# Kernel tuning notes

Hardware: AMD Instinct MI355X
Metric: run time of the kernel (lower is better)

The kernel has to match this reference:

```python
import jax, jax.numpy as jnp
import numpy as np

U_NUM, I_NUM, F_DIM, N_EDGES, BATCH = 50000, 20000, 64, 1000000, 131072
T = 1.0  # temperature

def setup_inputs() -> dict:
    key = jax.random.key(0)
    ks = jax.random.split(key, 16)
    return {
        'embed_user': jax.random.normal(ks[0], (U_NUM, F_DIM), jnp.float32) * 0.01,
        'embed_item': jax.random.normal(ks[1], (I_NUM, F_DIM), jnp.float32) * 0.01,
        'old_U_emb': jax.random.normal(ks[2], (U_NUM, F_DIM), jnp.float32),
        'old_I_emb': jax.random.normal(ks[3], (I_NUM, F_DIM), jnp.float32),
        'edge_rows': jax.random.randint(ks[4], (N_EDGES,), 0, U_NUM, jnp.int32),
        'edge_cols': jax.random.randint(ks[5], (N_EDGES,), 0, I_NUM, jnp.int32),
        'ui_vals': jax.random.uniform(ks[6], (N_EDGES,), jnp.float32),
        'iu_vals': jax.random.uniform(ks[7], (N_EDGES,), jnp.float32),
        'user': jax.random.randint(ks[8], (BATCH,), 0, U_NUM, jnp.int32),
        'item_i': jax.random.randint(ks[9], (BATCH,), 0, U_NUM, jnp.int32),
        'item_j': jax.random.randint(ks[10], (BATCH,), 0, U_NUM, jnp.int32),
        'degree_U': jax.random.uniform(ks[11], (BATCH,), jnp.float32),
        'item_z_U': jax.random.randint(ks[12], (BATCH,), 0, U_NUM, jnp.int32),
        'user_': jax.random.randint(ks[13], (BATCH,), 0, I_NUM, jnp.int32),
        'item_i_': jax.random.randint(ks[14], (BATCH,), 0, I_NUM, jnp.int32),
        'item_j_': jax.random.randint(ks[15], (BATCH,), 0, I_NUM, jnp.int32),
        'degree_I': jax.random.uniform(jax.random.fold_in(key, 99), (BATCH,), jnp.float32),
        'item_z_I': jax.random.randint(jax.random.fold_in(key, 98), (BATCH,), 0, I_NUM, jnp.int32),
    }

def _spmm_ui(vals, rows, cols, item_emb):
    # (U x I sparse) @ item_emb -> [U, F]
    return jax.ops.segment_sum(vals[:, None] * item_emb[cols], rows, num_segments=U_NUM)

def _spmm_iu(vals, rows, cols, user_emb):
    # (I x U sparse) @ user_emb -> [I, F]
    return jax.ops.segment_sum(vals[:, None] * user_emb[rows], cols, num_segments=I_NUM)

def _contrastive(idx_u, idx_i, idx_j, degree, num, old_emb, gcn_emb):
    u = old_emb[idx_u]            # [B, F]
    pi = gcn_emb[idx_i]           # [B, F]
    pj = gcn_emb[idx_j]           # [B, F]
    si = jnp.sum(u * pi, axis=-1) / T
    sj = jnp.sum(u * pj, axis=-1) / T
    # -log(exp(si) / (exp(sj) + exp(si))) = logaddexp(si, sj) - si  (stable form)
    log_ratio = si - jnp.logaddexp(si, sj)
    return -jnp.sum(log_ratio * degree) / num

def reference(embed_user, embed_item, old_U_emb, old_I_emb, ui_vals, iu_vals,
              degree_U, degree_I, edge_rows, edge_cols,
              user, item_i, item_j, item_z_U, user_, item_i_, item_j_, item_z_I):
    u0, i0 = embed_user, embed_item
    u1 = _spmm_ui(ui_vals, edge_rows, edge_cols, i0)
    i1 = _spmm_iu(iu_vals, edge_rows, edge_cols, u0)
    u2 = _spmm_ui(ui_vals, edge_rows, edge_cols, i1)
    i2 = _spmm_iu(iu_vals, edge_rows, edge_cols, u1)
    u3 = _spmm_ui(ui_vals, edge_rows, edge_cols, i2)
    i3 = _spmm_iu(iu_vals, edge_rows, edge_cols, u2)
    gcn_u = u0 + 0.5 * u1 + (1.0 / 3.0) * u2 + 0.25 * u3
    gcn_i = i0 + 0.5 * i1 + (1.0 / 3.0) * i2 + 0.25 * i3
    loss = _contrastive(user, item_i, item_j, degree_U, U_NUM, old_U_emb, gcn_u)
    loss = loss + _contrastive(user_, item_i_, item_j_, degree_I, I_NUM, old_I_emb, gcn_i)
    return loss
```

## Files before the change

kernel.cpp:

```cpp
#include <hip/hip_runtime.h>

#define U_NUM 50000
#define I_NUM 20000
#define F_DIM 64
#define N_EDGES 1000000
#define BATCH 131072

#define P_U 25
#define P_I 20
#define CAPP_U 45056
#define CAPP_I 55296
#define FP_U 200
#define FP_I 160
#define CAPF_U 5632
#define CAPF_I 6912
#define BRU 40
#define BRI 50
#define P1B 977

#if defined(__has_builtin)
#if __has_builtin(__builtin_amdgcn_cvt_pk_f32_fp8) && __has_builtin(__builtin_amdgcn_cvt_pk_fp8_f32)
#define HW_FP8 1
#endif
#endif

typedef float v2f __attribute__((ext_vector_type(2)));

__device__ __forceinline__ void dec4(unsigned u, float* f) {
#ifdef HW_FP8
    v2f lo = __builtin_amdgcn_cvt_pk_f32_fp8((int)u, false);
    v2f hi = __builtin_amdgcn_cvt_pk_f32_fp8((int)u, true);
    f[0] = lo.x; f[1] = lo.y; f[2] = hi.x; f[3] = hi.y;
#else
    #pragma unroll
    for (int i = 0; i < 4; i++) {
        unsigned v = (u >> (8 * i)) & 0xFFu;
        unsigned s = v >> 7, e = (v >> 3) & 15u, m = v & 7u;
        float mag = (e == 0) ? (float)m * 0.001953125f
                             : __uint_as_float(((e + 120u) << 23) | (m << 20));
        f[i] = s ? -mag : mag;
    }
#endif
}

#ifndef HW_FP8
__device__ __forceinline__ unsigned char enc1(float x) {
    unsigned s = (__float_as_uint(x) >> 31) << 7;
    float a = fabsf(x);
    if (a >= 448.f) return (unsigned char)(s | 0x7E);
    if (a < 0.015625f) {
        int m = __float2int_rn(a * 512.f);
        if (m >= 8) return (unsigned char)(s | 0x08);
        return (unsigned char)(s | m);
    }
    unsigned au = __float_as_uint(a);
    au += 0x7FFFFu + ((au >> 20) & 1u);
    int e = (int)(au >> 23) - 127;
    if (e > 8) return (unsigned char)(s | 0x7E);
    return (unsigned char)(s | ((unsigned)(e + 7) << 3) | ((au >> 20) & 7u));
}
#endif

__device__ __forceinline__ unsigned enc4(float a, float b, float c, float d) {
#ifdef HW_FP8
    int v = __builtin_amdgcn_cvt_pk_fp8_f32(a, b, 0, false);
    v = __builtin_amdgcn_cvt_pk_fp8_f32(c, d, v, true);
    return (unsigned)v;
#else
    return (unsigned)enc1(a) | ((unsigned)enc1(b) << 8)
         | ((unsigned)enc1(c) << 16) | ((unsigned)enc1(d) << 24);
#endif
}

__device__ __forceinline__ unsigned short f2b(float f) {
    unsigned b = __float_as_uint(f);
    b += 0x7FFFu + ((b >> 16) & 1u);
    return (unsigned short)(b >> 16);
}

#define N_EU 800000
#define N_EI 320000
#define N_OU 800000
#define N_OI 320000
__global__ void pass1_cvt(const int* __restrict__ rows, const int* __restrict__ cols,
                          const float* __restrict__ uiv, const float* __restrict__ iuv,
                          int* __restrict__ pcurU, int* __restrict__ pcurI,
                          int2* __restrict__ cbufU, int2* __restrict__ cbufI,
                          const float* __restrict__ eU, const float* __restrict__ eI,
                          const float* __restrict__ oU, const float* __restrict__ oI,
                          unsigned* __restrict__ e8U, unsigned* __restrict__ e8I,
                          unsigned* __restrict__ o8U, unsigned* __restrict__ o8I)
{
    if (blockIdx.x >= P1B) {
        int idx = (blockIdx.x - P1B) * 256 + threadIdx.x;
        const float* s; unsigned* d; int off; float sc;
        if (idx < N_EU)                        { s = eU; d = e8U; off = idx; sc = 128.f; }
        else if (idx < N_EU + N_EI)            { s = eI; d = e8I; off = idx - N_EU; sc = 128.f; }
        else if (idx < N_EU + N_EI + N_OU)     { s = oU; d = o8U; off = idx - N_EU - N_EI; sc = 1.f; }
        else if (idx < N_EU + N_EI + N_OU + N_OI) { s = oI; d = o8I; off = idx - N_EU - N_EI - N_OU; sc = 1.f; }
        else return;
        float4 v = ((const float4*)s)[off];
        d[off] = enc4(v.x * sc, v.y * sc, v.z * sc, v.w * sc);
        return;
    }

    __shared__ int histU[32], histI[32];
    __shared__ int lbaseU[32], lbaseI[32];
    __shared__ int deltaU[32], deltaI[32];
    __shared__ int totU, totI;
    __shared__ int2 recU[1024], recI[1024];
    __shared__ unsigned char pidU[1024], pidI[1024];

    if (threadIdx.x < 32) { histU[threadIdx.x] = 0; histI[threadIdx.x] = 0; }
    __syncthreads();

    int base = blockIdx.x * 1024;
    int r[4], c[4], lpU[4], lpI[4];
    float vu[4], vi[4];
    #pragma unroll
    for (int i = 0; i < 4; i++) {
        int e = base + threadIdx.x + i * 256;
        if (e < N_EDGES) {
            r[i] = rows[e]; c[i] = cols[e];
            vu[i] = uiv[e]; vi[i] = iuv[e];
            lpU[i] = atomicAdd(&histU[r[i] >> 11], 1);
            lpI[i] = atomicAdd(&histI[c[i] >> 10], 1);
        } else {
            lpU[i] = -1; lpI[i] = -1; r[i] = 0; c[i] = 0; vu[i] = 0.f; vi[i] = 0.f;
        }
    }
    __syncthreads();

    int lane = threadIdx.x & 63;
    int w    = threadIdx.x >> 6;
    if (w == 0) {
        int h = (lane < 32) ? histU[lane] : 0;
        int res = (lane < 32 && h) ? atomicAdd(&pcurU[lane], h) : 0;
        int inc = h;
        #pragma unroll
        for (int off = 1; off < 32; off <<= 1) {
            int t = __shfl_up(inc, off, 64);
            if (lane >= off) inc += t;
        }
        if (lane < 32) {
            int lb = inc - h;
            lbaseU[lane] = lb;
            deltaU[lane] = lane * CAPP_U + res - lb;
            if (lane == 31) totU = inc;
        }
    } else if (w == 1) {
        int h = (lane < 32) ? histI[lane] : 0;
        int res = (lane < 32 && h) ? atomicAdd(&pcurI[lane], h) : 0;
        int inc = h;
        #pragma unroll
        for (int off = 1; off < 32; off <<= 1) {
            int t = __shfl_up(inc, off, 64);
            if (lane >= off) inc += t;
        }
        if (lane < 32) {
            int lb = inc - h;
            lbaseI[lane] = lb;
            deltaI[lane] = lane * CAPP_I + res - lb;
            if (lane == 31) totI = inc;
        }
    }
    __syncthreads();

    #pragma unroll
    for (int i = 0; i < 4; i++) {
        if (lpU[i] >= 0) {
            int p = r[i] >> 11;
            int slot = lbaseU[p] + lpU[i];
            int2 rec;
            rec.x = (int)(((unsigned)c[i] << 16) | (unsigned)r[i]);
            rec.y = __float_as_int(vu[i]);
            recU[slot] = rec;
            pidU[slot] = (unsigned char)p;

            p = c[i] >> 10;
            slot = lbaseI[p] + lpI[i];
            rec.x = (int)(((unsigned)r[i] << 16) | (unsigned)c[i]);
            rec.y = __float_as_int(vi[i]);
            recI[slot] = rec;
            pidI[slot] = (unsigned char)p;
        }
    }
    __syncthreads();

    for (int t = threadIdx.x; t < totU; t += 256) {
        int p = pidU[t];
        int a = deltaU[p] + t;
        if (a < (p + 1) * CAPP_U) cbufU[a] = recU[t];
    }
    for (int t = threadIdx.x; t < totI; t += 256) {
        int p = pidI[t];
        int a = deltaI[p] + t;
        if (a < (p + 1) * CAPP_I) cbufI[a] = recI[t];
    }
}

__global__ void refine(const int* __restrict__ pcurU, const int2* __restrict__ cbufU,
                       int* __restrict__ fcurU, int2* __restrict__ fbufU,
                       const int* __restrict__ pcurI, const int2* __restrict__ cbufI,
                       int* __restrict__ fcurI, int2* __restrict__ fbufI)
{
    const int* pcur; const int2* cbuf; int* fcur; int2* fbuf;
    int p, b, br, capp, capf, shift;
    if (blockIdx.x < P_U * BRU) {
        pcur = pcurU; cbuf = cbufU; fcur = fcurU; fbuf = fbufU;
        p = blockIdx.x / BRU; b = blockIdx.x % BRU; br = BRU;
        capp = CAPP_U; capf = CAPF_U; shift = 8;
    } else {
        int q = blockIdx.x - P_U * BRU;
        pcur = pcurI; cbuf = cbufI; fcur = fcurI; fbuf = fbufI;
        p = q / BRI; b = q % BRI; br = BRI;
        capp = CAPP_I; capf = CAPF_I; shift = 7;
    }
    int n = min(pcur[p], capp);
    const int2* src = cbuf + (size_t)p * capp;

    __shared__ int hist[8], lbase[8], delta[8];
    __shared__ int tot;
    __shared__ int2 rec[1024];
    __shared__ unsigned char pid[1024];

    for (int base = b * 1024; base < n; base += br * 1024) {
        __syncthreads();
        if (threadIdx.x < 8) hist[threadIdx.x] = 0;
        __syncthreads();
        int2 rr[4]; int ff[4], lp[4];
        #pragma unroll
        for (int i = 0; i < 4; i++) {
            int t = base + i * 256 + threadIdx.x;
            if (t < n) {
                rr[i] = src[t];
                ff[i] = (int)((((unsigned)rr[i].x & 0xFFFFu) >> shift) & 7u);
                lp[i] = atomicAdd(&hist[ff[i]], 1);
            } else lp[i] = -1;
        }
        __syncthreads();
        if ((threadIdx.x >> 6) == 0) {
            int lane = threadIdx.x & 63;
            int h = (lane < 8) ? hist[lane] : 0;
            int res = (lane < 8 && h) ? atomicAdd(&fcur[p * 8 + lane], h) : 0;
            int inc = h;
            #pragma unroll
            for (int off = 1; off < 8; off <<= 1) {
                int t = __shfl_up(inc, off, 64);
                if (lane >= off) inc += t;
            }
            if (lane < 8) {
                int lb = inc - h;
                lbase[lane] = lb;
                delta[lane] = (p * 8 + lane) * capf + res - lb;
                if (lane == 7) tot = inc;
            }
        }
        __syncthreads();
        #pragma unroll
        for (int i = 0; i < 4; i++) {
            if (lp[i] >= 0) {
                int slot = lbase[ff[i]] + lp[i];
                rec[slot] = rr[i];
                pid[slot] = (unsigned char)ff[i];
            }
        }
        __syncthreads();
        for (int t = threadIdx.x; t < tot; t += 256) {
            int f2 = pid[t];
            int a = delta[f2] + t;
            if (a < (p * 8 + f2 + 1) * capf) fbuf[a] = rec[t];
        }
    }
}

__global__ void sort_csr(const int* __restrict__ fcurU, const int2* __restrict__ fbufU,
                         int* __restrict__ ptrU, int* __restrict__ cntU, unsigned* __restrict__ edgesU,
                         const int* __restrict__ fcurI, const int2* __restrict__ fbufI,
                         int* __restrict__ ptrI, int* __restrict__ cntI, unsigned* __restrict__ edgesI)
{
    __shared__ int hist[256], scan[256], curs[256];
    __shared__ int gbase_s;

    const int* fcur; const int2* fbuf; int* ptr; int* cnt; unsigned* edges;
    int fp, bins, capf, nrow;
    if (blockIdx.x < FP_U) {
        fcur = fcurU; fbuf = fbufU; ptr = ptrU; cnt = cntU; edges = edgesU;
        fp = blockIdx.x; bins = 256; capf = CAPF_U; nrow = U_NUM;
    } else {
        fcur = fcurI; fbuf = fbufI; ptr = ptrI; cnt = cntI; edges = edgesI;
        fp = blockIdx.x - FP_U; bins = 128; capf = CAPF_I; nrow = I_NUM;
    }

    if (threadIdx.x == 0) gbase_s = 0;
    for (int i = threadIdx.x; i < bins; i += 256) hist[i] = 0;
    __syncthreads();

    int contrib = ((int)threadIdx.x < fp) ? min(fcur[threadIdx.x], capf) : 0;
    #pragma unroll
    for (int off = 32; off > 0; off >>= 1) contrib += __shfl_down(contrib, off, 64);
    if ((threadIdx.x & 63) == 0 && contrib) atomicAdd(&gbase_s, contrib);

    int n = min(fcur[fp], capf);
    const int2* src = fbuf + (size_t)fp * capf;
    int mask = bins - 1;

    for (int t = threadIdx.x; t < n; t += 256) {
        int dst = src[t].x & 0xFFFF;
        atomicAdd(&hist[dst & mask], 1);
    }
    __syncthreads();

    int v = ((int)threadIdx.x < bins) ? hist[threadIdx.x] : 0;
    scan[threadIdx.x] = v;
    __syncthreads();
    for (int off = 1; off < 256; off <<= 1) {
        int t = ((int)threadIdx.x >= off) ? scan[threadIdx.x - off] : 0;
        __syncthreads();
        scan[threadIdx.x] += t;
        __syncthreads();
    }
    int ex = scan[threadIdx.x] - v;
    curs[threadIdx.x] = ex;
    __syncthreads();
    int gbase = gbase_s;

    if ((int)threadIdx.x < bins) {
        int row = fp * bins + threadIdx.x;
        if (row < nrow) {
            ptr[row] = gbase + ex;
            cnt[row] = v;
        }
    }

    for (int t = threadIdx.x; t < n; t += 256) {
        int2 r = src[t];
        int dst = r.x & 0xFFFF;
        int pos = atomicAdd(&curs[dst & mask], 1);
        unsigned rec = ((unsigned)f2b(__int_as_float(r.y)) << 16)
                     | ((unsigned)r.x >> 16);
        edges[gbase + pos] = rec;
    }
}

template <int MODE>
__global__ void spmm_level(const int* __restrict__ ptrU, const int* __restrict__ cntU,
                           const unsigned* __restrict__ edgesU, const unsigned* __restrict__ srcU,
                           unsigned* __restrict__ dstU,
                           const unsigned* __restrict__ l0U, const unsigned* __restrict__ l1U,
                           const unsigned* __restrict__ l2U, unsigned* __restrict__ g8U,
                           const int* __restrict__ ptrI, const int* __restrict__ cntI,
                           const unsigned* __restrict__ edgesI, const unsigned* __restrict__ srcI,
                           unsigned* __restrict__ dstI,
                           const unsigned* __restrict__ l0I, const unsigned* __restrict__ l1I,
                           const unsigned* __restrict__ l2I, unsigned* __restrict__ g8I)
{
    int wave = (blockIdx.x * blockDim.x + threadIdx.x) >> 6;
    bool isU = wave < U_NUM;
    int row = isU ? wave : wave - U_NUM;
    if (!isU && row >= I_NUM) return;

    const int*  ptr   = isU ? ptrU   : ptrI;
    const int*  cnt   = isU ? cntU   : cntI;
    const unsigned* edges = isU ? edgesU : edgesI;
    const unsigned* semb  = isU ? srcU   : srcI;

    int lane = threadIdx.x & 63;
    int sub  = lane >> 4;
    int q    = lane & 15;
    int begin = __builtin_amdgcn_readfirstlane(ptr[row]);
    int len   = __builtin_amdgcn_readfirstlane(cnt[row]);
    const unsigned* erow = edges + begin;

    float4 a0 = make_float4(0.f, 0.f, 0.f, 0.f);
    float4 a1 = make_float4(0.f, 0.f, 0.f, 0.f);
    float4 a2 = make_float4(0.f, 0.f, 0.f, 0.f);
    float4 a3 = make_float4(0.f, 0.f, 0.f, 0.f);
    int k = sub;
    for (; k + 12 < len; k += 16) {
        unsigned r0 = erow[k];
        unsigned r1 = erow[k + 4];
        unsigned r2 = erow[k + 8];
        unsigned r3 = erow[k + 12];
        unsigned x0 = semb[((size_t)(r0 & 0xFFFFu) << 4) + q];
        unsigned x1 = semb[((size_t)(r1 & 0xFFFFu) << 4) + q];
        unsigned x2 = semb[((size_t)(r2 & 0xFFFFu) << 4) + q];
        unsigned x3 = semb[((size_t)(r3 & 0xFFFFu) << 4) + q];
        float v0 = __uint_as_float(r0 & 0xFFFF0000u);
        float v1 = __uint_as_float(r1 & 0xFFFF0000u);
        float v2 = __uint_as_float(r2 & 0xFFFF0000u);
        float v3 = __uint_as_float(r3 & 0xFFFF0000u);
        float f0[4], f1[4], f2[4], f3[4];
        dec4(x0, f0); dec4(x1, f1); dec4(x2, f2); dec4(x3, f3);
        a0.x += v0 * f0[0]; a0.y += v0 * f0[1]; a0.z += v0 * f0[2]; a0.w += v0 * f0[3];
        a1.x += v1 * f1[0]; a1.y += v1 * f1[1]; a1.z += v1 * f1[2]; a1.w += v1 * f1[3];
        a2.x += v2 * f2[0]; a2.y += v2 * f2[1]; a2.z += v2 * f2[2]; a2.w += v2 * f2[3];
        a3.x += v3 * f3[0]; a3.y += v3 * f3[1]; a3.z += v3 * f3[2]; a3.w += v3 * f3[3];
    }
    for (; k < len; k += 4) {
        unsigned r0 = erow[k];
        unsigned x0 = semb[((size_t)(r0 & 0xFFFFu) << 4) + q];
        float v0 = __uint_as_float(r0 & 0xFFFF0000u);
        float f0[4];
        dec4(x0, f0);
        a0.x += v0 * f0[0]; a0.y += v0 * f0[1]; a0.z += v0 * f0[2]; a0.w += v0 * f0[3];
    }
    float4 acc;
    acc.x = (a0.x + a1.x) + (a2.x + a3.x);
    acc.y = (a0.y + a1.y) + (a2.y + a3.y);
    acc.z = (a0.z + a1.z) + (a2.z + a3.z);
    acc.w = (a0.w + a1.w) + (a2.w + a3.w);

    acc.x += __shfl_xor(acc.x, 16, 64);
    acc.y += __shfl_xor(acc.y, 16, 64);
    acc.z += __shfl_xor(acc.z, 16, 64);
    acc.w += __shfl_xor(acc.w, 16, 64);
    acc.x += __shfl_xor(acc.x, 32, 64);
    acc.y += __shfl_xor(acc.y, 32, 64);
    acc.z += __shfl_xor(acc.z, 32, 64);
    acc.w += __shfl_xor(acc.w, 32, 64);

    if (sub == 0) {
        size_t ro = ((size_t)row << 4) + q;
        if (MODE < 2) {
            unsigned* dst = isU ? dstU : dstI;
            dst[ro] = enc4(acc.x, acc.y, acc.z, acc.w);
        } else {
            const unsigned* l0 = isU ? l0U : l0I;
            const unsigned* l1 = isU ? l1U : l1I;
            const unsigned* l2 = isU ? l2U : l2I;
            unsigned* g8       = isU ? g8U : g8I;
            float e[4], b[4], c[4];
            dec4(l0[ro], e); dec4(l1[ro], b); dec4(l2[ro], c);
            const float third = 1.f / 3.f;
            float gx = 0.125f * (e[0] + 0.5f * b[0] + third * c[0] + 0.25f * acc.x);
            float gy = 0.125f * (e[1] + 0.5f * b[1] + third * c[1] + 0.25f * acc.y);
            float gz = 0.125f * (e[2] + 0.5f * b[2] + third * c[2] + 0.25f * acc.z);
            float gw = 0.125f * (e[3] + 0.5f * b[3] + third * c[3] + 0.25f * acc.w);
            g8[ro] = enc4(gx, gy, gz, gw);
        }
    }
}

__device__ __forceinline__ float dotq(const float* a, const float* b) {
    return a[0] * b[0] + a[1] * b[1] + a[2] * b[2] + a[3] * b[3];
}

__global__ void __launch_bounds__(256, 2)
contrastive_both(const unsigned* __restrict__ oldU, const unsigned* __restrict__ gcnU,
                 const int* __restrict__ userU, const int* __restrict__ iiU,
                 const int* __restrict__ ijU, const float* __restrict__ degU,
                 const unsigned* __restrict__ oldI, const unsigned* __restrict__ gcnI,
                 const int* __restrict__ userI, const int* __restrict__ iiI,
                 const int* __restrict__ ijI, const float* __restrict__ degI,
                 float* __restrict__ out)
{
    int lane = threadIdx.x & 63;
    int sub  = lane >> 4;
    int ql   = lane & 15;
    int qg = (blockIdx.x * blockDim.x + threadIdx.x) >> 4;
    int s0 = qg << 2;

    int sel = ql >> 2, so = s0 + (ql & 3);
    const int* pu = (sel == 0) ? (userU + so) : (sel == 1) ? (iiU + so)
                  : (sel == 2) ? (ijU + so)   : ((const int*)degU + so);
    const int* pi = (sel == 0) ? (userI + so) : (sel == 1) ? (iiI + so)
                  : (sel == 2) ? (ijI + so)   : ((const int*)degI + so);
    int idxU = *pu;
    int idxI = *pi;

    int qb = sub << 4;
    unsigned Au[4], Ai[4], Aj[4], Bu[4], Bi[4], Bj[4];
    #pragma unroll
    for (int t = 0; t < 4; t++) {
        int uU = __shfl(idxU, qb + t, 64);
        int iU = __shfl(idxU, qb + 4 + t, 64);
        int jU = __shfl(idxU, qb + 8 + t, 64);
        int uI = __shfl(idxI, qb + t, 64);
        int iI = __shfl(idxI, qb + 4 + t, 64);
        int jI = __shfl(idxI, qb + 8 + t, 64);
        Au[t] = oldU[((size_t)uU << 4) + ql];
        Ai[t] = gcnU[((size_t)iU << 4) + ql];
        Aj[t] = gcnU[((size_t)jU << 4) + ql];
        Bu[t] = oldI[((size_t)uI << 4) + ql];
        Bi[t] = gcnI[((size_t)iI << 4) + ql];
        Bj[t] = gcnI[((size_t)jI << 4) + ql];
    }

    float siU[4], sjU[4], siI[4], sjI[4];
    #pragma unroll
    for (int t = 0; t < 4; t++) {
        float fu[4], fi[4], fj[4];
        dec4(Au[t], fu); dec4(Ai[t], fi); dec4(Aj[t], fj);
        siU[t] = dotq(fu, fi); sjU[t] = dotq(fu, fj);
        dec4(Bu[t], fu); dec4(Bi[t], fi); dec4(Bj[t], fj);
        siI[t] = dotq(fu, fi); sjI[t] = dotq(fu, fj);
    }

    #pragma unroll
    for (int off = 1; off < 16; off <<= 1) {
        #pragma unroll
        for (int t = 0; t < 4; t++) {
            siU[t] += __shfl_xor(siU[t], off, 64);
            sjU[t] += __shfl_xor(sjU[t], off, 64);
            siI[t] += __shfl_xor(siI[t], off, 64);
            sjI[t] += __shfl_xor(sjI[t], off, 64);
        }
    }

    int t3 = ql & 3;
    bool isI = (ql & 4) != 0;
    float si = isI ? siI[t3] : siU[t3];
    float sj = isI ? sjI[t3] : sjU[t3];
    float dg = __int_as_float(__shfl(isI ? idxI : idxU, qb + 12 + t3, 64));
    float inv = isI ? (1.f / I_NUM) : (1.f / U_NUM);

    const float S = 0.0625f;
    si *= S; sj *= S;
    float m = fmaxf(si, sj);
    float lse = m + logf(expf(si - m) + expf(sj - m));
    float acc = (ql < 8) ? -(si - lse) * dg * inv : 0.f;

    #pragma unroll
    for (int off = 32; off > 0; off >>= 1) acc += __shfl_down(acc, off, 64);
    __shared__ float wsum[4];
    if (lane == 0) wsum[threadIdx.x >> 6] = acc;
    __syncthreads();
    if (threadIdx.x == 0)
        atomicAdd(out, wsum[0] + wsum[1] + wsum[2] + wsum[3]);
}

extern "C" void kernel_launch(void* const* d_in, const int* in_sizes, int n_in,
                              void* d_out, int out_size, void* d_ws, size_t ws_size,
                              hipStream_t stream)
{
    const float* embed_user = (const float*)d_in[0];
    const float* embed_item = (const float*)d_in[1];
    const float* old_U      = (const float*)d_in[2];
    const float* old_I      = (const float*)d_in[3];
    const int*   erow       = (const int*)d_in[4];
    const int*   ecol       = (const int*)d_in[5];
    const float* ui_vals    = (const float*)d_in[6];
    const float* iu_vals    = (const float*)d_in[7];
    const int*   user       = (const int*)d_in[8];
    const int*   item_i     = (const int*)d_in[9];
    const int*   item_j     = (const int*)d_in[10];
    const float* degU       = (const float*)d_in[11];
    const int*   user_      = (const int*)d_in[13];
    const int*   item_i_    = (const int*)d_in[14];
    const int*   item_j_    = (const int*)d_in[15];
    const float* degI       = (const float*)d_in[16];

    const size_t UF = (size_t)U_NUM * F_DIM;
    const size_t IF = (size_t)I_NUM * F_DIM;
    const size_t CREC = (size_t)P_U * CAPP_U + (size_t)P_I * CAPP_I;

    int2*  cbufU  = (int2*)d_ws;
    int2*  cbufI  = cbufU + (size_t)P_U * CAPP_U;
    unsigned* edgesU = (unsigned*)d_ws;
    unsigned* edgesI = edgesU + N_EDGES;
    int2*  fbufU  = (int2*)d_ws + CREC;
    int2*  fbufI  = fbufU + (size_t)FP_U * CAPF_U;
    char* cur = (char*)d_ws + 2 * CREC * sizeof(int2);
    unsigned* e8U = (unsigned*)cur; cur += UF;
    unsigned* e8I = (unsigned*)cur; cur += IF;
    unsigned* o8U = (unsigned*)cur; cur += UF;
    unsigned* o8I = (unsigned*)cur; cur += IF;
    unsigned* u1_8 = (unsigned*)cur; cur += UF;
    unsigned* u2_8 = (unsigned*)cur; cur += UF;
    unsigned* i1_8 = (unsigned*)cur; cur += IF;
    unsigned* i2_8 = (unsigned*)cur; cur += IF;
    unsigned* g8U  = (unsigned*)cur; cur += UF;
    unsigned* g8I  = (unsigned*)cur; cur += IF;
    int* pcurU = (int*)cur;
    int* pcurI = pcurU + 32;
    int* fcurU = pcurI + 32;
    int* fcurI = fcurU + 256;
    int* ptrU  = fcurI + 256;
    int* cntUa = ptrU + U_NUM;
    int* ptrI  = cntUa + U_NUM;
    int* cntIa = ptrI + I_NUM;

    dim3 blk(256);
    const int cv_blocks  = (N_EU + N_EI + N_OU + N_OI + 255) / 256;
    const int p1_blocks  = P1B + cv_blocks;
    const int rf_blocks  = P_U * BRU + P_I * BRI;
    const int st_blocks  = FP_U + FP_I;
    const int spmm_blocks = (U_NUM + I_NUM) / 4;

    hipMemsetAsync(pcurU, 0, 576 * sizeof(int), stream);
    hipMemsetAsync(d_out, 0, sizeof(float), stream);

    pass1_cvt<<<p1_blocks, blk, 0, stream>>>(erow, ecol, ui_vals, iu_vals,
                                             pcurU, pcurI, cbufU, cbufI,
                                             embed_user, embed_item, old_U, old_I,
                                             e8U, e8I, o8U, o8I);
    refine<<<rf_blocks, blk, 0, stream>>>(pcurU, cbufU, fcurU, fbufU,
                                          pcurI, cbufI, fcurI, fbufI);
    sort_csr<<<st_blocks, blk, 0, stream>>>(fcurU, fbufU, ptrU, cntUa, edgesU,
                                            fcurI, fbufI, ptrI, cntIa, edgesI);

    spmm_level<0><<<spmm_blocks, blk, 0, stream>>>(
        ptrU, cntUa, edgesU, e8I, u1_8, nullptr, nullptr, nullptr, nullptr,
        ptrI, cntIa, edgesI, e8U, i1_8, nullptr, nullptr, nullptr, nullptr);
    spmm_level<1><<<spmm_blocks, blk, 0, stream>>>(
        ptrU, cntUa, edgesU, i1_8, u2_8, nullptr, nullptr, nullptr, nullptr,
        ptrI, cntIa, edgesI, u1_8, i2_8, nullptr, nullptr, nullptr, nullptr);
    spmm_level<2><<<spmm_blocks, blk, 0, stream>>>(
        ptrU, cntUa, edgesU, i2_8, nullptr, e8U, u1_8, u2_8, g8U,
        ptrI, cntIa, edgesI, u2_8, nullptr, e8I, i1_8, i2_8, g8I);

    contrastive_both<<<2048, blk, 0, stream>>>(o8U, g8U, user, item_i, item_j, degU,
                                               o8I, g8I, user_, item_i_, item_j_, degI,
                                               (float*)d_out);
}
```

Baseline: 307.1 us.

## Replace two-pass coarse/refine edge bucketing with single-pass fine binning

Merges the coarse partition pass and the refine pass into one kernel. Each block takes an 8192-edge tile, builds a 256-bin shared-memory histogram, scans it, and scatters records straight into the fine bins. This drops the intermediate coarse buffer, which was written once and read back, and removes one kernel launch. The fp8 conversion work moves to a grid-stride loop over 512 blocks. The cost is fewer, larger blocks with 72KB of shared memory each, which lowers occupancy, plus more shared-memory atomic contention.

New measurement: 304.8 us. No clear change (-0.8%).

```diff
diff --git a/kernel.cpp b/kernel.cpp
--- a/kernel.cpp
+++ b/kernel.cpp
@@ -6,17 +6,14 @@
 #define N_EDGES 1000000
 #define BATCH 131072
 
-#define P_U 25
-#define P_I 20
-#define CAPP_U 45056
-#define CAPP_I 55296
 #define FP_U 200
 #define FP_I 160
 #define CAPF_U 5632
 #define CAPF_I 6912
-#define BRU 40
-#define BRI 50
-#define P1B 977
+#define TILE 8192
+#define NBU 123
+#define NBI 123
+#define CVB 512
 
 #if defined(__has_builtin)
 #if __has_builtin(__builtin_amdgcn_cvt_pk_f32_fp8) && __has_builtin(__builtin_amdgcn_cvt_pk_fp8_f32)
@@ -82,195 +79,89 @@
 #define N_EI 320000
 #define N_OU 800000
 #define N_OI 320000
-__global__ void pass1_cvt(const int* __restrict__ rows, const int* __restrict__ cols,
-                          const float* __restrict__ uiv, const float* __restrict__ iuv,
-                          int* __restrict__ pcurU, int* __restrict__ pcurI,
-                          int2* __restrict__ cbufU, int2* __restrict__ cbufI,
-                          const float* __restrict__ eU, const float* __restrict__ eI,
-                          const float* __restrict__ oU, const float* __restrict__ oI,
-                          unsigned* __restrict__ e8U, unsigned* __restrict__ e8I,
-                          unsigned* __restrict__ o8U, unsigned* __restrict__ o8I)
+#define CVT_TOT (N_EU + N_EI + N_OU + N_OI)
+__global__ void build_fine(const int* __restrict__ rows, const int* __restrict__ cols,
+                           const float* __restrict__ uiv, const float* __restrict__ iuv,
+                           int* __restrict__ fcurU, int2* __restrict__ fbufU,
+                           int* __restrict__ fcurI, int2* __restrict__ fbufI,
+                           const float* __restrict__ eU, const float* __restrict__ eI,
+                           const float* __restrict__ oU, const float* __restrict__ oI,
+                           unsigned* __restrict__ e8U, unsigned* __restrict__ e8I,
+                           unsigned* __restrict__ o8U, unsigned* __restrict__ o8I)
 {
-    if (blockIdx.x >= P1B) {
-        int idx = (blockIdx.x - P1B) * 256 + threadIdx.x;
-        const float* s; unsigned* d; int off; float sc;
-        if (idx < N_EU)                        { s = eU; d = e8U; off = idx; sc = 128.f; }
-        else if (idx < N_EU + N_EI)            { s = eI; d = e8I; off = idx - N_EU; sc = 128.f; }
-        else if (idx < N_EU + N_EI + N_OU)     { s = oU; d = o8U; off = idx - N_EU - N_EI; sc = 1.f; }
-        else if (idx < N_EU + N_EI + N_OU + N_OI) { s = oI; d = o8I; off = idx - N_EU - N_EI - N_OU; sc = 1.f; }
-        else return;
-        float4 v = ((const float4*)s)[off];
-        d[off] = enc4(v.x * sc, v.y * sc, v.z * sc, v.w * sc);
+    if (blockIdx.x >= NBU + NBI) {
+        for (int idx = (blockIdx.x - NBU - NBI) * 256 + threadIdx.x;
+             idx < CVT_TOT; idx += CVB * 256) {
+            const float* s; unsigned* d; int off; float sc;
+            if (idx < N_EU)                      { s = eU; d = e8U; off = idx; sc = 128.f; }
+            else if (idx < N_EU + N_EI)          { s = eI; d = e8I; off = idx - N_EU; sc = 128.f; }
+            else if (idx < N_EU + N_EI + N_OU)   { s = oU; d = o8U; off = idx - N_EU - N_EI; sc = 1.f; }
+            else                                 { s = oI; d = o8I; off = idx - N_EU - N_EI - N_OU; sc = 1.f; }
+            float4 v = ((const float4*)s)[off];
+            d[off] = enc4(v.x * sc, v.y * sc, v.z * sc, v.w * sc);
+        }
         return;
     }
 
-    __shared__ int histU[32], histI[32];
-    __shared__ int lbaseU[32], lbaseI[32];
-    __shared__ int deltaU[32], deltaI[32];
-    __shared__ int totU, totI;
-    __shared__ int2 recU[1024], recI[1024];
-    __shared__ unsigned char pidU[1024], pidI[1024];
-
-    if (threadIdx.x < 32) { histU[threadIdx.x] = 0; histI[threadIdx.x] = 0; }
-    __syncthreads();
-
-    int base = blockIdx.x * 1024;
-    int r[4], c[4], lpU[4], lpI[4];
-    float vu[4], vi[4];
-    #pragma unroll
-    for (int i = 0; i < 4; i++) {
-        int e = base + threadIdx.x + i * 256;
-        if (e < N_EDGES) {
-            r[i] = rows[e]; c[i] = cols[e];
-            vu[i] = uiv[e]; vi[i] = iuv[e];
-            lpU[i] = atomicAdd(&histU[r[i] >> 11], 1);
-            lpI[i] = atomicAdd(&histI[c[i] >> 10], 1);
-        } else {
-            lpU[i] = -1; lpI[i] = -1; r[i] = 0; c[i] = 0; vu[i] = 0.f; vi[i] = 0.f;
-        }
-    }
-    __syncthreads();
-
-    int lane = threadIdx.x & 63;
-    int w    = threadIdx.x >> 6;
-    if (w == 0) {
-        int h = (lane < 32) ? histU[lane] : 0;
-        int res = (lane < 32 && h) ? atomicAdd(&pcurU[lane], h) : 0;
-        int inc = h;
-        #pragma unroll
-        for (int off = 1; off < 32; off <<= 1) {
-            int t = __shfl_up(inc, off, 64);
-            if (lane >= off) inc += t;
-        }
-        if (lane < 32) {
-            int lb = inc - h;
-            lbaseU[lane] = lb;
-            deltaU[lane] = lane * CAPP_U + res - lb;
-            if (lane == 31) totU = inc;
-        }
-    } else if (w == 1) {
-        int h = (lane < 32) ? histI[lane] : 0;
-        int res = (lane < 32 && h) ? atomicAdd(&pcurI[lane], h) : 0;
-        int inc = h;
-        #pragma unroll
-        for (int off = 1; off < 32; off <<= 1) {
-            int t = __shfl_up(inc, off, 64);
-            if (lane >= off) inc += t;
-        }
-        if (lane < 32) {
-            int lb = inc - h;
-            lbaseI[lane] = lb;
-            deltaI[lane] = lane * CAPP_I + res - lb;
-            if (lane == 31) totI = inc;
-        }
-    }
-    __syncthreads();
-
-    #pragma unroll
-    for (int i = 0; i < 4; i++) {
-        if (lpU[i] >= 0) {
-            int p = r[i] >> 11;
-            int slot = lbaseU[p] + lpU[i];
-            int2 rec;
-            rec.x = (int)(((unsigned)c[i] << 16) | (unsigned)r[i]);
-            rec.y = __float_as_int(vu[i]);
-            recU[slot] = rec;
-            pidU[slot] = (unsigned char)p;
-
-            p = c[i] >> 10;
-            slot = lbaseI[p] + lpI[i];
-            rec.x = (int)(((unsigned)r[i] << 16) | (unsigned)c[i]);
-            rec.y = __float_as_int(vi[i]);
-            recI[slot] = rec;
-            pidI[slot] = (unsigned char)p;
-        }
-    }
-    __syncthreads();
-
-    for (int t = threadIdx.x; t < totU; t += 256) {
-        int p = pidU[t];
-        int a = deltaU[p] + t;
-        if (a < (p + 1) * CAPP_U) cbufU[a] = recU[t];
-    }
-    for (int t = threadIdx.x; t < totI; t += 256) {
-        int p = pidI[t];
-        int a = deltaI[p] + t;
-        if (a < (p + 1) * CAPP_I) cbufI[a] = recI[t];
-    }
-}
-
-__global__ void refine(const int* __restrict__ pcurU, const int2* __restrict__ cbufU,
-                       int* __restrict__ fcurU, int2* __restrict__ fbufU,
-                       const int* __restrict__ pcurI, const int2* __restrict__ cbufI,
-                       int* __restrict__ fcurI, int2* __restrict__ fbufI)
-{
-    const int* pcur; const int2* cbuf; int* fcur; int2* fbuf;
-    int p, b, br, capp, capf, shift;
-    if (blockIdx.x < P_U * BRU) {
-        pcur = pcurU; cbuf = cbufU; fcur = fcurU; fbuf = fbufU;
-        p = blockIdx.x / BRU; b = blockIdx.x % BRU; br = BRU;
-        capp = CAPP_U; capf = CAPF_U; shift = 8;
-    } else {
-        int q = blockIdx.x - P_U * BRU;
-        pcur = pcurI; cbuf = cbufI; fcur = fcurI; fbuf = fbufI;
-        p = q / BRI; b = q % BRI; br = BRI;
-        capp = CAPP_I; capf = CAPF_I; shift = 7;
-    }
-    int n = min(pcur[p], capp);
-    const int2* src = cbuf + (size_t)p * capp;
-
-    __shared__ int hist[8], lbase[8], delta[8];
-    __shared__ int tot;
-    __shared__ int2 rec[1024];
-    __shared__ unsigned char pid[1024];
-
-    for (int base = b * 1024; base < n; base += br * 1024) {
+    __shared__ int2 rec[TILE];
+    __shared__ unsigned char pid[TILE];
+    __shared__ int hist[256], scan[256], curs[256], delta[256];
+
+    bool isU = blockIdx.x < NBU;
+    int tb = isU ? blockIdx.x : blockIdx.x - NBU;
+    int n0 = tb * TILE;
+    int n  = min(TILE, N_EDGES - n0);
+    int bins  = isU ? FP_U : FP_I;
+    int capf  = isU ? CAPF_U : CAPF_I;
+    int shift = isU ? 8 : 7;
+    int* fcur = isU ? fcurU : fcurI;
+    int2* fbuf = isU ? fbufU : fbufI;
+    const int* keys = isU ? rows : cols;
+    const int* srcs = isU ? cols : rows;
+    const float* vals = isU ? uiv : iuv;
+
+    hist[threadIdx.x] = 0;
+    __syncthreads();
+
+    for (int t = threadIdx.x; t < n; t += 256)
+        atomicAdd(&hist[keys[n0 + t] >> shift], 1);
+    __syncthreads();
+
+    int v = hist[threadIdx.x];
+    scan[threadIdx.x] = v;
+    __syncthreads();
+    for (int off = 1; off < 256; off <<= 1) {
+        int t = ((int)threadIdx.x >= off) ? scan[threadIdx.x - off] : 0;
         __syncthreads();
-        if (threadIdx.x < 8) hist[threadIdx.x] = 0;
+        scan[threadIdx.x] += t;
         __syncthreads();
-        int2 rr[4]; int ff[4], lp[4];
-        #pragma unroll
-        for (int i = 0; i < 4; i++) {
-            int t = base + i * 256 + threadIdx.x;
-            if (t < n) {
-                rr[i] = src[t];
-                ff[i] = (int)((((unsigned)rr[i].x & 0xFFFFu) >> shift) & 7u);
-                lp[i] = atomicAdd(&hist[ff[i]], 1);
-            } else lp[i] = -1;
-        }
-        __syncthreads();
-        if ((threadIdx.x >> 6) == 0) {
-            int lane = threadIdx.x & 63;
-            int h = (lane < 8) ? hist[lane] : 0;
-            int res = (lane < 8 && h) ? atomicAdd(&fcur[p * 8 + lane], h) : 0;
-            int inc = h;
-            #pragma unroll
-            for (int off = 1; off < 8; off <<= 1) {
-                int t = __shfl_up(inc, off, 64);
-                if (lane >= off) inc += t;
-            }
-            if (lane < 8) {
-                int lb = inc - h;
-                lbase[lane] = lb;
-                delta[lane] = (p * 8 + lane) * capf + res - lb;
-                if (lane == 7) tot = inc;
-            }
-        }
-        __syncthreads();
-        #pragma unroll
-        for (int i = 0; i < 4; i++) {
-            if (lp[i] >= 0) {
-                int slot = lbase[ff[i]] + lp[i];
-                rec[slot] = rr[i];
-                pid[slot] = (unsigned char)ff[i];
-            }
-        }
-        __syncthreads();
-        for (int t = threadIdx.x; t < tot; t += 256) {
-            int f2 = pid[t];
-            int a = delta[f2] + t;
-            if (a < (p * 8 + f2 + 1) * capf) fbuf[a] = rec[t];
-        }
+    }
+    int lbase = scan[threadIdx.x] - v;
+    curs[threadIdx.x] = lbase;
+    if ((int)threadIdx.x < bins) {
+        int res = v ? atomicAdd(&fcur[threadIdx.x], v) : 0;
+        delta[threadIdx.x] = threadIdx.x * capf + res - lbase;
+    }
+    __syncthreads();
+
+    for (int t = threadIdx.x; t < n; t += 256) {
+        int key = keys[n0 + t];
+        int src = srcs[n0 + t];
+        float vv = vals[n0 + t];
+        int b = key >> shift;
+        int slot = atomicAdd(&curs[b], 1);
+        int2 r;
+        r.x = (int)(((unsigned)src << 16) | (unsigned)key);
+        r.y = __float_as_int(vv);
+        rec[slot] = r;
+        pid[slot] = (unsigned char)b;
+    }
+    __syncthreads();
+
+    for (int t = threadIdx.x; t < n; t += 256) {
+        int b = pid[t];
+        int a = delta[b] + t;
+        if (a < (b + 1) * capf) fbuf[a] = rec[t];
     }
 }
 
@@ -553,15 +444,14 @@
 
     const size_t UF = (size_t)U_NUM * F_DIM;
     const size_t IF = (size_t)I_NUM * F_DIM;
-    const size_t CREC = (size_t)P_U * CAPP_U + (size_t)P_I * CAPP_I;
-
-    int2*  cbufU  = (int2*)d_ws;
-    int2*  cbufI  = cbufU + (size_t)P_U * CAPP_U;
-    unsigned* edgesU = (unsigned*)d_ws;
+    const size_t FRECU = (size_t)FP_U * CAPF_U;
+    const size_t FRECI = (size_t)FP_I * CAPF_I;
+
+    int2*  fbufU  = (int2*)d_ws;
+    int2*  fbufI  = fbufU + FRECU;
+    unsigned* edgesU = (unsigned*)(fbufI + FRECI);
     unsigned* edgesI = edgesU + N_EDGES;
-    int2*  fbufU  = (int2*)d_ws + CREC;
-    int2*  fbufI  = fbufU + (size_t)FP_U * CAPF_U;
-    char* cur = (char*)d_ws + 2 * CREC * sizeof(int2);
+    char* cur = (char*)(edgesI + N_EDGES);
     unsigned* e8U = (unsigned*)cur; cur += UF;
     unsigned* e8I = (unsigned*)cur; cur += IF;
     unsigned* o8U = (unsigned*)cur; cur += UF;
@@ -572,9 +462,7 @@
     unsigned* i2_8 = (unsigned*)cur; cur += IF;
     unsigned* g8U  = (unsigned*)cur; cur += UF;
     unsigned* g8I  = (unsigned*)cur; cur += IF;
-    int* pcurU = (int*)cur;
-    int* pcurI = pcurU + 32;
-    int* fcurU = pcurI + 32;
+    int* fcurU = (int*)cur;
     int* fcurI = fcurU + 256;
     int* ptrU  = fcurI + 256;
     int* cntUa = ptrU + U_NUM;
@@ -582,21 +470,17 @@
     int* cntIa = ptrI + I_NUM;
 
     dim3 blk(256);
-    const int cv_blocks  = (N_EU + N_EI + N_OU + N_OI + 255) / 256;
-    const int p1_blocks  = P1B + cv_blocks;
-    const int rf_blocks  = P_U * BRU + P_I * BRI;
+    const int bf_blocks  = NBU + NBI + CVB;
     const int st_blocks  = FP_U + FP_I;
     const int spmm_blocks = (U_NUM + I_NUM) / 4;
 
-    hipMemsetAsync(pcurU, 0, 576 * sizeof(int), stream);
+    hipMemsetAsync(fcurU, 0, 512 * sizeof(int), stream);
     hipMemsetAsync(d_out, 0, sizeof(float), stream);
 
-    pass1_cvt<<<p1_blocks, blk, 0, stream>>>(erow, ecol, ui_vals, iu_vals,
-                                             pcurU, pcurI, cbufU, cbufI,
-                                             embed_user, embed_item, old_U, old_I,
-                                             e8U, e8I, o8U, o8I);
-    refine<<<rf_blocks, blk, 0, stream>>>(pcurU, cbufU, fcurU, fbufU,
-                                          pcurI, cbufI, fcurI, fbufI);
+    build_fine<<<bf_blocks, blk, 0, stream>>>(erow, ecol, ui_vals, iu_vals,
+                                              fcurU, fbufU, fcurI, fbufI,
+                                              embed_user, embed_item, old_U, old_I,
+                                              e8U, e8I, o8U, o8I);
     sort_csr<<<st_blocks, blk, 0, stream>>>(fcurU, fbufU, ptrU, cntUa, edgesU,
                                             fcurI, fbufI, ptrI, cntIa, edgesI);
 
```
